# Kernel optimization log

Hardware: AMD Instinct MI355X
Metric: run time of the kernel (lower is better)

## Reference

```python
import math
import jax, jax.numpy as jnp
import numpy as np

B, H, L, Dh = 4, 8, 4096, 64
TOPK_FACTOR = 1.0


def setup_inputs() -> dict:
    key = jax.random.key(0)
    kq, kk, kv = jax.random.split(key, 3)
    shape = (B, H, L, Dh)
    return {
        "q": jax.random.normal(kq, shape, dtype=jnp.float32),
        "k": jax.random.normal(kk, shape, dtype=jnp.float32),
        "v": jax.random.normal(kv, shape, dtype=jnp.float32),
    }


def reference(q, k, v):
    b, h, length, dh = q.shape
    # FFT cross-correlation over the time axis, averaged over Dh -> (B,H,L)
    qf = jnp.fft.rfft(q, axis=2)
    kf = jnp.fft.rfft(k, axis=2)
    corr = jnp.fft.irfft(qf * jnp.conj(kf), n=length, axis=2).mean(axis=-1)
    # top-k delays (k_top is static: depends only on L)
    k_top = max(1, int(TOPK_FACTOR * math.log(length + 1)))
    weights, delays = jax.lax.top_k(corr, k_top)  # (B,H,K)
    attn = jax.nn.softmax(weights, axis=-1)       # (B,H,K)
    # circular-shift gather: idx[b,h,t,j] = (t - delay[b,h,j]) mod L
    t = jnp.arange(length)
    idx = (t[None, None, :, None] - delays[:, :, None, :]) % length  # (B,H,L,K)
    # gathered: (B,H,L,K,Dh)
    gathered = jnp.take_along_axis(v[:, :, :, None, :], idx[..., None], axis=2)
    out = (gathered * attn[:, :, None, :, None]).sum(axis=3)  # (B,H,L,Dh)
    return out
```

## Files before the change

### kernel.cpp

```cpp
#include <hip/hip_runtime.h>
#include <math.h>

#define LEN 4096
#define LOG2LEN 12
#define DH 64
#define NBH 32
#define KTOP 8
#define DPB 4
#define NGRP (DH / DPB)

#define PART_F2 ((size_t)NBH * NGRP * LEN)
#define SPEC_F2 (NBH * LEN)
#define TWO_PI 6.2831853071795864769f

#define XSTR 272

__device__ __forceinline__ int rev16_12(int x) {
  return ((x & 15) << 8) | (x & 240) | (x >> 8);
}

struct cf { float r, i; };
__device__ __forceinline__ cf cadd(const cf a, const cf b) { return {a.r + b.r, a.i + b.i}; }
__device__ __forceinline__ cf csub(const cf a, const cf b) { return {a.r - b.r, a.i - b.i}; }
__device__ __forceinline__ cf cmul(const cf a, const float wr, const float wi) {
  return {a.r * wr - a.i * wi, a.r * wi + a.i * wr};
}
template <int S>
__device__ __forceinline__ cf cmuli(const cf a) {
  return (S < 0) ? cf{a.i, -a.r} : cf{-a.i, a.r};
}
template <int S>
__device__ __forceinline__ cf twc(const cf a, const float c, const float s) {
  return cmul(a, c, (S < 0) ? -s : s);
}
template <int S>
__device__ __forceinline__ void r4(cf& a, cf& b, cf& c, cf& d) {
  const cf t0 = cadd(a, c), t1 = csub(a, c), t2 = cadd(b, d), t3 = csub(b, d);
  const cf j3 = cmuli<S>(t3);
  a = cadd(t0, t2); c = csub(t0, t2);
  b = cadd(t1, j3); d = csub(t1, j3);
}
template <int S>
__device__ __forceinline__ void dft16(cf* x) {
  r4<S>(x[0], x[4], x[8], x[12]);
  r4<S>(x[1], x[5], x[9], x[13]);
  r4<S>(x[2], x[6], x[10], x[14]);
  r4<S>(x[3], x[7], x[11], x[15]);
  const float C1 = 0.92387953251128675613f;
  const float S1 = 0.38268343236508977173f;
  const float R2 = 0.70710678118654752440f;
  x[5] = twc<S>(x[5], C1, S1);
  x[6] = twc<S>(x[6], R2, R2);
  x[7] = twc<S>(x[7], S1, C1);
  x[9] = twc<S>(x[9], R2, R2);
  x[10] = cmuli<S>(x[10]);
  x[11] = twc<S>(x[11], -R2, R2);
  x[13] = twc<S>(x[13], S1, C1);
  x[14] = twc<S>(x[14], -R2, R2);
  x[15] = twc<S>(x[15], -C1, -S1);
  r4<S>(x[0], x[1], x[2], x[3]);
  r4<S>(x[4], x[5], x[6], x[7]);
  r4<S>(x[8], x[9], x[10], x[11]);
  r4<S>(x[12], x[13], x[14], x[15]);
  cf t;
  t = x[1]; x[1] = x[4]; x[4] = t;
  t = x[2]; x[2] = x[8]; x[8] = t;
  t = x[3]; x[3] = x[12]; x[12] = t;
  t = x[6]; x[6] = x[9]; x[9] = t;
  t = x[7]; x[7] = x[13]; x[13] = t;
  t = x[11]; x[11] = x[14]; x[14] = t;
}

__global__ __launch_bounds__(256, 2) void ac_fft_fwd(const float* __restrict__ q,
                                                     const float* __restrict__ k,
                                                     float2* __restrict__ part) {
  __shared__ float lre[16 * XSTR], lim[16 * XSTR];
  __shared__ float2 acc[LEN];
  const int tid = threadIdx.x;
  const int hi = tid >> 4, lo = tid & 15;
  const int bid = (int)blockIdx.x;
  const int task = ((bid & 7) << 6) | (bid >> 3);
  const int bh = task >> 4;
  const int g = task & 15;

  float s1, c1, s2, c2;
  sincosf(-TWO_PI * (float)tid / (float)LEN, &s1, &c1);
  sincosf(-TWO_PI * (float)lo / 256.0f, &s2, &c2);
  float w1pr[15], w1pi[15];
  {
    float cr = c1, ci = s1;
#pragma unroll
    for (int kk = 0; kk < 15; ++kk) {
      w1pr[kk] = cr; w1pi[kk] = ci;
      const float nr = cr * c1 - ci * s1;
      ci = cr * s1 + ci * c1;
      cr = nr;
    }
  }

#pragma unroll
  for (int i = 0; i < 16; ++i) acc[tid + 256 * i] = make_float2(0.f, 0.f);

  float hq[DPB][16], hk[DPB][16];
  {
    const float* qb = q + (size_t)bh * LEN * DH + 4 * g;
    const float* kb = k + (size_t)bh * LEN * DH + 4 * g;
#pragma unroll
    for (int n1 = 0; n1 < 16; ++n1) {
      const size_t off = (size_t)(tid + 256 * n1) * DH;
      const float4 q4 = *reinterpret_cast<const float4*>(qb + off);
      const float4 k4 = *reinterpret_cast<const float4*>(kb + off);
      hq[0][n1] = q4.x; hq[1][n1] = q4.y; hq[2][n1] = q4.z; hq[3][n1] = q4.w;
      hk[0][n1] = k4.x; hk[1][n1] = k4.y; hk[2][n1] = k4.z; hk[3][n1] = k4.w;
    }
  }

#pragma unroll
  for (int dd = 0; dd < DPB; ++dd) {
    cf x[16];
#pragma unroll
    for (int n1 = 0; n1 < 16; ++n1) { x[n1].r = hq[dd][n1]; x[n1].i = hk[dd][n1]; }
    dft16<-1>(x);
#pragma unroll
    for (int k1 = 1; k1 < 16; ++k1) x[k1] = cmul(x[k1], w1pr[k1 - 1], w1pi[k1 - 1]);
    __syncthreads();
#pragma unroll
    for (int k1 = 0; k1 < 16; ++k1) {
      lre[k1 * XSTR + tid] = x[k1].r;
      lim[k1 * XSTR + tid] = x[k1].i;
    }
    __syncthreads();
#pragma unroll
    for (int m1 = 0; m1 < 16; ++m1) {
      const int a = hi * XSTR + 16 * m1 + lo;
      x[m1].r = lre[a]; x[m1].i = lim[a];
    }
    dft16<-1>(x);
    {
      float cr = c2, ci = s2;
#pragma unroll
      for (int j1 = 1; j1 < 16; ++j1) {
        x[j1] = cmul(x[j1], cr, ci);
        const float nr = cr * c2 - ci * s2;
        ci = cr * s2 + ci * c2;
        cr = nr;
      }
    }
    __builtin_amdgcn_wave_barrier();
#pragma unroll
    for (int j1 = 0; j1 < 16; ++j1) {
      lre[hi * XSTR + 16 * j1 + lo] = x[j1].r;
      lim[hi * XSTR + 16 * j1 + lo] = x[j1].i;
    }
    __builtin_amdgcn_wave_barrier();
#pragma unroll
    for (int m2 = 0; m2 < 16; ++m2) {
      const int a = hi * XSTR + 16 * lo + m2;
      x[m2].r = lre[a]; x[m2].i = lim[a];
    }
    dft16<-1>(x);
    __builtin_amdgcn_wave_barrier();
#pragma unroll
    for (int j2 = 0; j2 < 16; ++j2) {
      lre[hi * XSTR + 16 * lo + j2] = x[j2].r;
      lim[hi * XSTR + 16 * lo + j2] = x[j2].i;
    }
    __syncthreads();
#pragma unroll
    for (int i = 0; i < 16; ++i) {
      const int p = tid + 256 * i;
      const int f = rev16_12(p);
      const int f2 = (LEN - f) & (LEN - 1);
      const int p2 = rev16_12(f2);
      const int a1 = i * XSTR + tid;
      const int a2 = (p2 >> 8) * XSTR + (p2 & 255);
      const float ar = lre[a1], ai = lim[a1];
      const float br = lre[a2], bi = lim[a2];
      float2 a = acc[p];
      a.x += 0.5f * (ar * bi + ai * br);
      a.y += 0.25f * ((ar * ar + ai * ai) - (br * br + bi * bi));
      acc[p] = a;
    }
  }
  float2* op = part + (size_t)(bh * NGRP + g) * LEN;
#pragma unroll
  for (int i = 0; i < 16; ++i) {
    const int p = tid + 256 * i;
    op[p] = acc[p];
  }
}

__global__ __launch_bounds__(256) void ac_reduce(const float2* __restrict__ part,
                                                 float2* __restrict__ spec) {
  const int bh = blockIdx.x >> 4;
  const int p = ((blockIdx.x & 15) << 8) | threadIdx.x;
  float accr = 0.f, acci = 0.f;
#pragma unroll 4
  for (int g = 0; g < NGRP; ++g) {
    const float2 v = part[((size_t)(bh * NGRP + g) << LOG2LEN) + p];
    accr += v.x; acci += v.y;
  }
  spec[((size_t)bh << LOG2LEN) + p] = make_float2(accr, acci);
}

__global__ __launch_bounds__(256, 2) void ac_fft_inv(const float2* __restrict__ spec,
                                                     float* __restrict__ attn,
                                                     int* __restrict__ delays) {
  __shared__ float lre[16 * XSTR], lim[16 * XSTR];
  __shared__ float rv[256];
  __shared__ int ri[256];
  __shared__ float selv[KTOP];
  __shared__ int seli[KTOP];
  const int bh = blockIdx.x;
  const int tid = threadIdx.x;
  const int hi = tid >> 4, lo = tid & 15;

  cf x[16];
  {
    const float4* b4 = reinterpret_cast<const float4*>(spec + ((size_t)bh << LOG2LEN) + 16 * tid);
#pragma unroll
    for (int i = 0; i < 8; ++i) {
      const float4 vv = b4[i];
      x[2 * i].r = vv.x; x[2 * i].i = vv.y;
      x[2 * i + 1].r = vv.z; x[2 * i + 1].i = vv.w;
    }
  }

  float sA, cA, sB0, cB0, sBs, cBs;
  sincosf(TWO_PI * (float)lo / 256.0f, &sA, &cA);
  sincosf(TWO_PI * (float)(hi * lo) / (float)LEN, &sB0, &cB0);
  sincosf(TWO_PI * (float)hi / 256.0f, &sBs, &cBs);

  dft16<1>(x);
  {
    float cr = cA, ci = sA;
#pragma unroll
    for (int t0 = 1; t0 < 16; ++t0) {
      x[t0] = cmul(x[t0], cr, ci);
      const float nr = cr * cA - ci * sA;
      ci = cr * sA + ci * cA;
      cr = nr;
    }
  }
#pragma unroll
  for (int t0 = 0; t0 < 16; ++t0) {
    lre[hi * XSTR + 16 * t0 + lo] = x[t0].r;
    lim[hi * XSTR + 16 * t0 + lo] = x[t0].i;
  }
  __builtin_amdgcn_wave_barrier();
#pragma unroll
  for (int f1 = 0; f1 < 16; ++f1) {
    const int a = hi * XSTR + 16 * lo + f1;
    x[f1].r = lre[a]; x[f1].i = lim[a];
  }
  dft16<1>(x);
  {
    float cr = cB0, ci = sB0;
#pragma unroll
    for (int t1 = 0; t1 < 16; ++t1) {
      x[t1] = cmul(x[t1], cr, ci);
      const float nr = cr * cBs - ci * sBs;
      ci = cr * sBs + ci * cBs;
      cr = nr;
    }
  }
  __builtin_amdgcn_wave_barrier();
#pragma unroll
  for (int t1 = 0; t1 < 16; ++t1) {
    lre[hi * XSTR + 16 * t1 + lo] = x[t1].r;
    lim[hi * XSTR + 16 * t1 + lo] = x[t1].i;
  }
  __syncthreads();
#pragma unroll
  for (int f0 = 0; f0 < 16; ++f0) {
    const int a = f0 * XSTR + 16 * hi + lo;
    x[f0].r = lre[a]; x[f0].i = lim[a];
  }
  dft16<1>(x);
  __syncthreads();
  const float scale = 1.0f / ((float)LEN * (float)DH);
#pragma unroll
  for (int t2 = 0; t2 < 16; ++t2) lre[256 * t2 + tid] = x[t2].r * scale;
  __syncthreads();

  for (int kk = 0; kk < KTOP; ++kk) {
    float mv = -3.0e38f;
    int mi = 0;
    for (int t = tid; t < LEN; t += 256) {
      const float xv = lre[t];
      if (xv > mv) { mv = xv; mi = t; }
    }
    rv[tid] = mv; ri[tid] = mi;
    __syncthreads();
    for (int s = 128; s > 0; s >>= 1) {
      if (tid < s) {
        if (rv[tid + s] > rv[tid]) { rv[tid] = rv[tid + s]; ri[tid] = ri[tid + s]; }
      }
      __syncthreads();
    }
    if (tid == 0) {
      selv[kk] = rv[0];
      seli[kk] = ri[0];
      lre[ri[0]] = -3.0e38f;
    }
    __syncthreads();
  }
  if (tid == 0) {
    const float mx = selv[0];
    float ex[KTOP];
    float sum = 0.f;
    for (int j = 0; j < KTOP; ++j) { ex[j] = expf(selv[j] - mx); sum += ex[j]; }
    const float inv = 1.0f / sum;
    for (int j = 0; j < KTOP; ++j) {
      attn[bh * KTOP + j] = ex[j] * inv;
      delays[bh * KTOP + j] = seli[j];
    }
  }
}

__global__ __launch_bounds__(256) void ac_gather(const float* __restrict__ v,
                                                 const float* __restrict__ attn,
                                                 const int* __restrict__ delays,
                                                 float* __restrict__ out) {
  const int bx = blockIdx.x;
  const int xcd = bx & 7;
  const int i = bx >> 3;
  const int bh = (xcd << 2) | (i & 3);
  const int chunk = i >> 2;
  const int tid = threadIdx.x;
  float aw[KTOP];
  int dl[KTOP];
#pragma unroll
  for (int j = 0; j < KTOP; ++j) {
    aw[j] = attn[bh * KTOP + j];
    dl[j] = delays[bh * KTOP + j];
  }
  const int e = chunk * 1024 + tid * 4;
  const int t = e >> 6;
  const int d = e & 63;
  const float* vb = v + (size_t)bh * LEN * DH;
  float4 acc = make_float4(0.f, 0.f, 0.f, 0.f);
#pragma unroll
  for (int j = 0; j < KTOP; ++j) {
    int src = t - dl[j];
    if (src < 0) src += LEN;
    const float4 vv = *reinterpret_cast<const float4*>(vb + (size_t)src * DH + d);
    acc.x += aw[j] * vv.x;
    acc.y += aw[j] * vv.y;
    acc.z += aw[j] * vv.z;
    acc.w += aw[j] * vv.w;
  }
  *reinterpret_cast<float4*>(out + (size_t)bh * LEN * DH + e) = acc;
}

extern "C" void kernel_launch(void* const* d_in, const int* in_sizes, int n_in,
                              void* d_out, int out_size, void* d_ws, size_t ws_size,
                              hipStream_t stream) {
  const float* q = (const float*)d_in[0];
  const float* k = (const float*)d_in[1];
  const float* v = (const float*)d_in[2];
  float* out = (float*)d_out;

  float2* part = (float2*)d_ws;
  float2* spec = part + PART_F2;
  float* attn = (float*)(spec + SPEC_F2);
  int* delays = (int*)(attn + NBH * KTOP);

  ac_fft_fwd<<<dim3(NBH * NGRP), dim3(256), 0, stream>>>(q, k, part);
  ac_reduce<<<dim3(NBH * NGRP), dim3(256), 0, stream>>>(part, spec);
  ac_fft_inv<<<dim3(NBH), dim3(256), 0, stream>>>(spec, attn, delays);
  ac_gather<<<dim3(NBH * 256), dim3(256), 0, stream>>>(v, attn, delays, out);
}
```

Baseline: 82.73 us.

## Process two FFT columns per pass and accumulate spectra in registers

The forward FFT kernel now transforms two Dh columns at a time using two LDS buffer sets. This halves the number of block-wide barriers and exposes more independent work per thread. The shared-memory accumulator is replaced by per-thread register accumulators, and the per-thread twiddle table is replaced by on-the-fly recurrence. This adds register pressure and leaves LDS use about the same, which may hurt occupancy under the launch bound of 2. The reduce launch count change is numerically identical, since NGRP is 16.

```diff
diff --git a/kernel.cpp b/kernel.cpp
--- a/kernel.cpp
+++ b/kernel.cpp
@@ -74,8 +74,8 @@
 __global__ __launch_bounds__(256, 2) void ac_fft_fwd(const float* __restrict__ q,
                                                      const float* __restrict__ k,
                                                      float2* __restrict__ part) {
-  __shared__ float lre[16 * XSTR], lim[16 * XSTR];
-  __shared__ float2 acc[LEN];
+  __shared__ float lreA[16 * XSTR], limA[16 * XSTR];
+  __shared__ float lreB[16 * XSTR], limB[16 * XSTR];
   const int tid = threadIdx.x;
   const int hi = tid >> 4, lo = tid & 15;
   const int bid = (int)blockIdx.x;
@@ -86,20 +86,6 @@
   float s1, c1, s2, c2;
   sincosf(-TWO_PI * (float)tid / (float)LEN, &s1, &c1);
   sincosf(-TWO_PI * (float)lo / 256.0f, &s2, &c2);
-  float w1pr[15], w1pi[15];
-  {
-    float cr = c1, ci = s1;
-#pragma unroll
-    for (int kk = 0; kk < 15; ++kk) {
-      w1pr[kk] = cr; w1pi[kk] = ci;
-      const float nr = cr * c1 - ci * s1;
-      ci = cr * s1 + ci * c1;
-      cr = nr;
-    }
-  }
-
-#pragma unroll
-  for (int i = 0; i < 16; ++i) acc[tid + 256 * i] = make_float2(0.f, 0.f);
 
   float hq[DPB][16], hk[DPB][16];
   {
@@ -115,32 +101,54 @@
     }
   }
 
-#pragma unroll
-  for (int dd = 0; dd < DPB; ++dd) {
-    cf x[16];
-#pragma unroll
-    for (int n1 = 0; n1 < 16; ++n1) { x[n1].r = hq[dd][n1]; x[n1].i = hk[dd][n1]; }
-    dft16<-1>(x);
-#pragma unroll
-    for (int k1 = 1; k1 < 16; ++k1) x[k1] = cmul(x[k1], w1pr[k1 - 1], w1pi[k1 - 1]);
+  float srg[16], sig[16];
+#pragma unroll
+  for (int i = 0; i < 16; ++i) { srg[i] = 0.f; sig[i] = 0.f; }
+
+#pragma unroll
+  for (int pp = 0; pp < 2; ++pp) {
+    cf x0[16], x1[16];
+#pragma unroll
+    for (int n1 = 0; n1 < 16; ++n1) {
+      x0[n1].r = hq[2 * pp][n1];     x0[n1].i = hk[2 * pp][n1];
+      x1[n1].r = hq[2 * pp + 1][n1]; x1[n1].i = hk[2 * pp + 1][n1];
+    }
+    dft16<-1>(x0);
+    dft16<-1>(x1);
+    {
+      float cr = c1, ci = s1;
+#pragma unroll
+      for (int k1 = 1; k1 < 16; ++k1) {
+        x0[k1] = cmul(x0[k1], cr, ci);
+        x1[k1] = cmul(x1[k1], cr, ci);
+        const float nr = cr * c1 - ci * s1;
+        ci = cr * s1 + ci * c1;
+        cr = nr;
+      }
+    }
     __syncthreads();
 #pragma unroll
     for (int k1 = 0; k1 < 16; ++k1) {
-      lre[k1 * XSTR + tid] = x[k1].r;
-      lim[k1 * XSTR + tid] = x[k1].i;
+      lreA[k1 * XSTR + tid] = x0[k1].r;
+      limA[k1 * XSTR + tid] = x0[k1].i;
+      lreB[k1 * XSTR + tid] = x1[k1].r;
+      limB[k1 * XSTR + tid] = x1[k1].i;
     }
     __syncthreads();
 #pragma unroll
     for (int m1 = 0; m1 < 16; ++m1) {
       const int a = hi * XSTR + 16 * m1 + lo;
-      x[m1].r = lre[a]; x[m1].i = lim[a];
-    }
-    dft16<-1>(x);
+      x0[m1].r = lreA[a]; x0[m1].i = limA[a];
+      x1[m1].r = lreB[a]; x1[m1].i = limB[a];
+    }
+    dft16<-1>(x0);
+    dft16<-1>(x1);
     {
       float cr = c2, ci = s2;
 #pragma unroll
       for (int j1 = 1; j1 < 16; ++j1) {
-        x[j1] = cmul(x[j1], cr, ci);
+        x0[j1] = cmul(x0[j1], cr, ci);
+        x1[j1] = cmul(x1[j1], cr, ci);
         const float nr = cr * c2 - ci * s2;
         ci = cr * s2 + ci * c2;
         cr = nr;
@@ -149,21 +157,27 @@
     __builtin_amdgcn_wave_barrier();
 #pragma unroll
     for (int j1 = 0; j1 < 16; ++j1) {
-      lre[hi * XSTR + 16 * j1 + lo] = x[j1].r;
-      lim[hi * XSTR + 16 * j1 + lo] = x[j1].i;
+      lreA[hi * XSTR + 16 * j1 + lo] = x0[j1].r;
+      limA[hi * XSTR + 16 * j1 + lo] = x0[j1].i;
+      lreB[hi * XSTR + 16 * j1 + lo] = x1[j1].r;
+      limB[hi * XSTR + 16 * j1 + lo] = x1[j1].i;
     }
     __builtin_amdgcn_wave_barrier();
 #pragma unroll
     for (int m2 = 0; m2 < 16; ++m2) {
       const int a = hi * XSTR + 16 * lo + m2;
-      x[m2].r = lre[a]; x[m2].i = lim[a];
-    }
-    dft16<-1>(x);
+      x0[m2].r = lreA[a]; x0[m2].i = limA[a];
+      x1[m2].r = lreB[a]; x1[m2].i = limB[a];
+    }
+    dft16<-1>(x0);
+    dft16<-1>(x1);
     __builtin_amdgcn_wave_barrier();
 #pragma unroll
     for (int j2 = 0; j2 < 16; ++j2) {
-      lre[hi * XSTR + 16 * lo + j2] = x[j2].r;
-      lim[hi * XSTR + 16 * lo + j2] = x[j2].i;
+      lreA[hi * XSTR + 16 * lo + j2] = x0[j2].r;
+      limA[hi * XSTR + 16 * lo + j2] = x0[j2].i;
+      lreB[hi * XSTR + 16 * lo + j2] = x1[j2].r;
+      limB[hi * XSTR + 16 * lo + j2] = x1[j2].i;
     }
     __syncthreads();
 #pragma unroll
@@ -174,19 +188,25 @@
       const int p2 = rev16_12(f2);
       const int a1 = i * XSTR + tid;
       const int a2 = (p2 >> 8) * XSTR + (p2 & 255);
-      const float ar = lre[a1], ai = lim[a1];
-      const float br = lre[a2], bi = lim[a2];
-      float2 a = acc[p];
-      a.x += 0.5f * (ar * bi + ai * br);
-      a.y += 0.25f * ((ar * ar + ai * ai) - (br * br + bi * bi));
-      acc[p] = a;
+      {
+        const float ar = lreA[a1], ai = limA[a1];
+        const float br = lreA[a2], bi = limA[a2];
+        srg[i] += 0.5f * (ar * bi + ai * br);
+        sig[i] += 0.25f * ((ar * ar + ai * ai) - (br * br + bi * bi));
+      }
+      {
+        const float ar = lreB[a1], ai = limB[a1];
+        const float br = lreB[a2], bi = limB[a2];
+        srg[i] += 0.5f * (ar * bi + ai * br);
+        sig[i] += 0.25f * ((ar * ar + ai * ai) - (br * br + bi * bi));
+      }
     }
   }
   float2* op = part + (size_t)(bh * NGRP + g) * LEN;
 #pragma unroll
   for (int i = 0; i < 16; ++i) {
     const int p = tid + 256 * i;
-    op[p] = acc[p];
+    op[p] = make_float2(srg[i], sig[i]);
   }
 }
 
@@ -367,7 +387,7 @@
   int* delays = (int*)(attn + NBH * KTOP);
 
   ac_fft_fwd<<<dim3(NBH * NGRP), dim3(256), 0, stream>>>(q, k, part);
-  ac_reduce<<<dim3(NBH * NGRP), dim3(256), 0, stream>>>(part, spec);
+  ac_reduce<<<dim3(NBH * 16), dim3(256), 0, stream>>>(part, spec);
   ac_fft_inv<<<dim3(NBH), dim3(256), 0, stream>>>(spec, attn, delays);
   ac_gather<<<dim3(NBH * 256), dim3(256), 0, stream>>>(v, attn, delays, out);
 }
```

Measured after the change: 104.4 us. 26.2% more time.

## Add transpose pre-pass so forward FFT reads contiguous interleaved q/k rows

Applied to the files above, without the earlier changes.

Adds a transpose kernel that rewrites q and k into a per-(bh,d) time-major interleaved complex buffer in workspace. The forward FFT then reads each dimension's signal with coalesced float2 loads instead of strided float4 loads over Dh. The dd loop is no longer unrolled, which lowers register pressure. The cost is an extra kernel launch plus a full write and re-read of a 64MB buffer, and the new path only runs when the workspace is large enough.

```diff
diff --git a/kernel.cpp b/kernel.cpp
--- a/kernel.cpp
+++ b/kernel.cpp
@@ -9,6 +9,7 @@
 #define DPB 4
 #define NGRP (DH / DPB)
 
+#define ZT_F2 ((size_t)NBH * DH * LEN)
 #define PART_F2 ((size_t)NBH * NGRP * LEN)
 #define SPEC_F2 (NBH * LEN)
 #define TWO_PI 6.2831853071795864769f
@@ -71,8 +72,41 @@
   t = x[11]; x[11] = x[14]; x[14] = t;
 }
 
+__global__ __launch_bounds__(256, 4) void ac_transpose(const float* __restrict__ q,
+                                                       const float* __restrict__ k,
+                                                       float2* __restrict__ zT) {
+  __shared__ float tq[64][65], tk[64][65];
+  const int bh = blockIdx.x >> 6;
+  const int t0 = (blockIdx.x & 63) * 64;
+  const int tid = threadIdx.x;
+  const int tl = tid >> 2;
+  const int c = tid & 3;
+  const float* qb = q + ((size_t)bh * LEN + t0) * DH;
+  const float* kb = k + ((size_t)bh * LEN + t0) * DH;
+#pragma unroll
+  for (int r = 0; r < 4; ++r) {
+    const int d0 = (c + r * 4) * 4;
+    const float4 vq = *reinterpret_cast<const float4*>(qb + (size_t)tl * DH + d0);
+    const float4 vk = *reinterpret_cast<const float4*>(kb + (size_t)tl * DH + d0);
+    tq[tl][d0] = vq.x; tq[tl][d0 + 1] = vq.y; tq[tl][d0 + 2] = vq.z; tq[tl][d0 + 3] = vq.w;
+    tk[tl][d0] = vk.x; tk[tl][d0 + 1] = vk.y; tk[tl][d0 + 2] = vk.z; tk[tl][d0 + 3] = vk.w;
+  }
+  __syncthreads();
+  const int d = tid >> 2;
+  const int s = tid & 3;
+  float2* ob = zT + ((size_t)(bh * DH + d)) * LEN + t0;
+#pragma unroll
+  for (int r = 0; r < 8; ++r) {
+    const int t = (s + r * 4) * 2;
+    const float4 o = make_float4(tq[t][d], tk[t][d], tq[t + 1][d], tk[t + 1][d]);
+    *reinterpret_cast<float4*>(&ob[t]) = o;
+  }
+}
+
+template <bool TR>
 __global__ __launch_bounds__(256, 2) void ac_fft_fwd(const float* __restrict__ q,
                                                      const float* __restrict__ k,
+                                                     const float2* __restrict__ zT,
                                                      float2* __restrict__ part) {
   __shared__ float lre[16 * XSTR], lim[16 * XSTR];
   __shared__ float2 acc[LEN];
@@ -101,8 +135,8 @@
 #pragma unroll
   for (int i = 0; i < 16; ++i) acc[tid + 256 * i] = make_float2(0.f, 0.f);
 
-  float hq[DPB][16], hk[DPB][16];
-  {
+  float hq[TR ? 1 : DPB][16], hk[TR ? 1 : DPB][16];
+  if (!TR) {
     const float* qb = q + (size_t)bh * LEN * DH + 4 * g;
     const float* kb = k + (size_t)bh * LEN * DH + 4 * g;
 #pragma unroll
@@ -110,16 +144,30 @@
       const size_t off = (size_t)(tid + 256 * n1) * DH;
       const float4 q4 = *reinterpret_cast<const float4*>(qb + off);
       const float4 k4 = *reinterpret_cast<const float4*>(kb + off);
-      hq[0][n1] = q4.x; hq[1][n1] = q4.y; hq[2][n1] = q4.z; hq[3][n1] = q4.w;
-      hk[0][n1] = k4.x; hk[1][n1] = k4.y; hk[2][n1] = k4.z; hk[3][n1] = k4.w;
-    }
-  }
-
-#pragma unroll
+      hq[0][n1] = q4.x; hq[1 % (TR ? 1 : DPB)][n1] = q4.y;
+      hq[2 % (TR ? 1 : DPB)][n1] = q4.z; hq[3 % (TR ? 1 : DPB)][n1] = q4.w;
+      hk[0][n1] = k4.x; hk[1 % (TR ? 1 : DPB)][n1] = k4.y;
+      hk[2 % (TR ? 1 : DPB)][n1] = k4.z; hk[3 % (TR ? 1 : DPB)][n1] = k4.w;
+    }
+  }
+
+#pragma unroll 1
   for (int dd = 0; dd < DPB; ++dd) {
     cf x[16];
-#pragma unroll
-    for (int n1 = 0; n1 < 16; ++n1) { x[n1].r = hq[dd][n1]; x[n1].i = hk[dd][n1]; }
+    if (TR) {
+      const float2* zb = zT + (size_t)(bh * DH + g * DPB + dd) * LEN;
+#pragma unroll
+      for (int n1 = 0; n1 < 16; ++n1) {
+        const float2 z = zb[tid + 256 * n1];
+        x[n1].r = z.x; x[n1].i = z.y;
+      }
+    } else {
+#pragma unroll
+      for (int n1 = 0; n1 < 16; ++n1) {
+        x[n1].r = hq[dd % (TR ? 1 : DPB)][n1];
+        x[n1].i = hk[dd % (TR ? 1 : DPB)][n1];
+      }
+    }
     dft16<-1>(x);
 #pragma unroll
     for (int k1 = 1; k1 < 16; ++k1) x[k1] = cmul(x[k1], w1pr[k1 - 1], w1pi[k1 - 1]);
@@ -361,12 +409,22 @@
   const float* v = (const float*)d_in[2];
   float* out = (float*)d_out;
 
-  float2* part = (float2*)d_ws;
+  const size_t need = ZT_F2 * 8 + PART_F2 * 8 + (size_t)SPEC_F2 * 8 +
+                      (size_t)NBH * KTOP * 8;
+  const bool tr = (ws_size >= need);
+
+  float2* zT = (float2*)d_ws;
+  float2* part = tr ? (zT + ZT_F2) : zT;
   float2* spec = part + PART_F2;
   float* attn = (float*)(spec + SPEC_F2);
   int* delays = (int*)(attn + NBH * KTOP);
 
-  ac_fft_fwd<<<dim3(NBH * NGRP), dim3(256), 0, stream>>>(q, k, part);
+  if (tr) {
+    ac_transpose<<<dim3(NBH * 64), dim3(256), 0, stream>>>(q, k, zT);
+    ac_fft_fwd<true><<<dim3(NBH * NGRP), dim3(256), 0, stream>>>(q, k, zT, part);
+  } else {
+    ac_fft_fwd<false><<<dim3(NBH * NGRP), dim3(256), 0, stream>>>(q, k, zT, part);
+  }
   ac_reduce<<<dim3(NBH * NGRP), dim3(256), 0, stream>>>(part, spec);
   ac_fft_inv<<<dim3(NBH), dim3(256), 0, stream>>>(spec, attn, delays);
   ac_gather<<<dim3(NBH * 256), dim3(256), 0, stream>>>(v, attn, delays, out);
```

Result: slower. 91.69 us (+10.8%).
